# Optimization experiments

Hardware: AMD Instinct MI355X
Metric: run time of the kernel (lower is better)

## Reference

```python
import jax, jax.numpy as jnp
import numpy as np

S, B, DIN, DBERT, H, L = 128, 32, 256, 768, 512, 2
NT_POS, NT_MORPH = 32, 64


def setup_inputs() -> dict:
    key = jax.random.key(0)
    ks = iter(jax.random.split(key, 32))
    def rn(shape, s=0.1):
        return jax.random.normal(next(ks), shape, dtype=jnp.float32) * s
    D0 = DIN + DBERT  # 1024 == 2*H, so per-layer LSTM weights stack cleanly
    return {
        "src_segments": rn((S, B, DIN), 1.0),
        "bert_encodings": rn((B, DBERT), 1.0),
        "labels_pos": jax.random.randint(next(ks), (S, B), 0, NT_POS, dtype=jnp.int32),
        "labels_morph": jax.random.randint(next(ks), (S, B), 0, NT_MORPH, dtype=jnp.int32),
        # stacked LSTM params: [layer, direction, ...], PyTorch gate order i,f,g,o
        "w_ih": rn((L, 2, 4 * H, D0)),
        "w_hh": rn((L, 2, 4 * H, H)),
        "b_ih": rn((L, 2, 4 * H)),
        "b_hh": rn((L, 2, 4 * H)),
        "head_w_pos": rn((NT_POS, 2 * H)),
        "head_b_pos": rn((NT_POS,)),
        "head_w_morph": rn((NT_MORPH, 2 * H)),
        "head_b_morph": rn((NT_MORPH,)),
        "start_pos": rn((NT_POS,)), "end_pos": rn((NT_POS,)), "trans_pos": rn((NT_POS, NT_POS)),
        "start_morph": rn((NT_MORPH,)), "end_morph": rn((NT_MORPH,)), "trans_morph": rn((NT_MORPH, NT_MORPH)),
    }


def _run_dir(x, w_ih, w_hh, b):
    # x: [S, B, D]; one LSTM direction via scan over time
    bsz, hd = x.shape[1], w_hh.shape[1]
    def step(carry, xt):
        h, c = carry
        g = xt @ w_ih.T + h @ w_hh.T + b  # [B, 4H]
        i, f, gg, o = jnp.split(g, 4, axis=-1)
        c = jax.nn.sigmoid(f) * c + jax.nn.sigmoid(i) * jnp.tanh(gg)
        h = jax.nn.sigmoid(o) * jnp.tanh(c)
        return (h, c), h
    init = (jnp.zeros((bsz, hd), x.dtype), jnp.zeros((bsz, hd), x.dtype))
    _, hs = jax.lax.scan(step, init, x)
    return hs


def _bilstm(x, w_ih, w_hh, b_ih, b_hh):
    out = x
    for l in range(w_ih.shape[0]):
        b = b_ih[l] + b_hh[l]
        fwd = _run_dir(out, w_ih[l, 0], w_hh[l, 0], b[0])
        bwd = _run_dir(out[::-1], w_ih[l, 1], w_hh[l, 1], b[1])[::-1]
        out = jnp.concatenate([fwd, bwd], axis=-1)  # [S, B, 2H]
    return out


def _crf_ll(em, tags, start, trans, end):
    # torchcrf log-likelihood, mask=None, reduction='sum'. em: [S,B,K], tags: [S,B]
    bsz = em.shape[1]
    first = start[tags[0]] + em[0, jnp.arange(bsz), tags[0]]
    em_sc = jnp.take_along_axis(em, tags[..., None], axis=2)[..., 0]  # [S,B]
    num = first + trans[tags[:-1], tags[1:]].sum(0) + em_sc[1:].sum(0) + end[tags[-1]]
    def step(alpha, et):  # alpha: [B,K]
        return jax.nn.logsumexp(alpha[:, :, None] + trans[None], axis=1) + et, None
    alpha, _ = jax.lax.scan(step, start[None, :] + em[0], em[1:])
    den = jax.nn.logsumexp(alpha + end[None, :], axis=1)
    return jnp.sum(num - den)


def reference(src_segments, bert_encodings, labels_pos, labels_morph,
              w_ih, w_hh, b_ih, b_hh,
              head_w_pos, head_b_pos, head_w_morph, head_b_morph,
              start_pos, end_pos, trans_pos, start_morph, end_morph, trans_morph):
    # bert encodings are repeated over seq and concatenated on features
    bert = jnp.broadcast_to(bert_encodings[None], (src_segments.shape[0],) + bert_encodings.shape)
    emb = jnp.concatenate([src_segments, bert], axis=-1)  # dropout p=0 -> identity
    out = _bilstm(emb, w_ih, w_hh, b_ih, b_hh)            # [S,B,2H]
    feat_pos = out @ head_w_pos.T + head_b_pos            # [S,B,32]
    feat_morph = out @ head_w_morph.T + head_b_morph      # [S,B,64]
    ll = (_crf_ll(feat_pos, labels_pos, start_pos, trans_pos, end_pos)
          + _crf_ll(feat_morph, labels_morph, start_morph, trans_morph, end_morph))
    return -ll  # loss = -sum_f crf_f(emissions_f, labels_f)
```

## Files before the change

kernel.cpp:

```cpp
#include <hip/hip_runtime.h>


typedef unsigned short u16;
typedef unsigned long long u64;
typedef __attribute__((ext_vector_type(8))) __bf16 bf16x8;
typedef __attribute__((ext_vector_type(4))) float floatx4;

static __device__ __forceinline__ u16 f2bf(float f) {
  unsigned int u = __float_as_uint(f);
  u += 0x7fffu + ((u >> 16) & 1u);
  return (u16)(u >> 16);
}
static __device__ __forceinline__ float sigf(float x) {
  return 1.0f / (1.0f + __expf(-x));
}
static __device__ __forceinline__ float tanh_(float x) {
  return 1.0f - 2.0f / (1.0f + __expf(2.0f * x));
}
static __device__ __forceinline__ floatx4 mfma16(bf16x8 a, bf16x8 b, floatx4 c) {
  return __builtin_amdgcn_mfma_f32_16x16x32_bf16(a, b, c, 0, 0, 0);
}

__global__ __launch_bounds__(256) void prep_kernel(
    const float* __restrict__ w_ih, const float* __restrict__ w_hh,
    const float* __restrict__ b_ih, const float* __restrict__ b_hh,
    const float* __restrict__ src,  const float* __restrict__ bert,
    const float* __restrict__ hwp,  const float* __restrict__ hbp,
    const float* __restrict__ hwm,  const float* __restrict__ hbm,
    u16* __restrict__ Wsrc, u16* __restrict__ Wbert, u16* __restrict__ Wih1,
    u16* __restrict__ Whh,  u16* __restrict__ SrcBf, u16* __restrict__ BertBf,
    u16* __restrict__ Wheads, float* __restrict__ b0sum, float* __restrict__ b1sum,
    float* __restrict__ hb, float* __restrict__ dout)
{
  const int NA = 4194304;
  const int NB = 4194304;
  const int NC = 4194304;
  const int ND = 1048576;
  const int NE = 24576;
  const int NF = 98304;
  const int NG = 8192;
  const int NH = 96;
  const int TOTAL = NA + NB + NC + ND + NE + NF + NG + NH + 1;
  for (int i = blockIdx.x * 256 + threadIdx.x; i < TOTAL; i += gridDim.x * 256) {
    int x = i;
    if (x < NA) {
      int c = x & 1023, r = x >> 10;
      float v = w_ih[x];
      if (c < 256) Wsrc[r * 256 + c] = f2bf(v);
      else         Wbert[r * 768 + (c - 256)] = f2bf(v);
      continue;
    }
    x -= NA;
    if (x < NB) { Wih1[x] = f2bf(w_ih[NA + x]); continue; }
    x -= NB;
    if (x < NC) { Whh[x] = f2bf(w_hh[x]); continue; }
    x -= NC;
    if (x < ND) { SrcBf[x] = f2bf(src[x]); continue; }
    x -= ND;
    if (x < NE) { BertBf[x] = f2bf(bert[x]); continue; }
    x -= NE;
    if (x < NF) {
      Wheads[x] = f2bf(x < 32768 ? hwp[x] : hwm[x - 32768]);
      continue;
    }
    x -= NF;
    if (x < NG) {
      float v = b_ih[x] + b_hh[x];
      if (x < 4096) b0sum[x] = v; else b1sum[x - 4096] = v;
      continue;
    }
    x -= NG;
    if (x < NH) { hb[x] = (x < 32) ? hbp[x] : hbm[x - 32]; continue; }
    dout[0] = 0.f;
  }
}

__global__ __launch_bounds__(256) void gemm_nt(
    const u16* __restrict__ A, int lda,
    const u16* __restrict__ B, int ldb,
    float* __restrict__ C, int ldc,
    int M, int N, int K,
    const float* __restrict__ bias_n,
    const float* __restrict__ auxBN, int auxld,
    int n_split, long dir_stride)
{
  __shared__ __align__(16) u16 As[128 * 64];
  __shared__ __align__(16) u16 Bs[128 * 64];
  const int m0 = blockIdx.y * 128, n0 = blockIdx.x * 128;
  const int tid = threadIdx.x;
  const int wv = tid >> 6, ln = tid & 63;
  const int wm = wv & 1, wn = wv >> 1;
  const int q = ln >> 4, l15 = ln & 15;
  floatx4 acc[4][4];
#pragma unroll
  for (int a = 0; a < 4; ++a)
#pragma unroll
    for (int b2 = 0; b2 < 4; ++b2) acc[a][b2] = (floatx4){0.f, 0.f, 0.f, 0.f};

  for (int kk = 0; kk < K; kk += 64) {
    __syncthreads();
#pragma unroll
    for (int j = 0; j < 4; ++j) {
      const int idx = j * 256 + tid;
      const int r = idx >> 3, cc = idx & 7;
      const int slot = cc ^ (r & 7);
      const int ra = min(m0 + r, M - 1);
      *(int4*)&As[r * 64 + slot * 8] = *(const int4*)&A[(long)ra * lda + kk + cc * 8];
      const int rb = min(n0 + r, N - 1);
      *(int4*)&Bs[r * 64 + slot * 8] = *(const int4*)&B[(long)rb * ldb + kk + cc * 8];
    }
    __syncthreads();
#pragma unroll
    for (int ks = 0; ks < 2; ++ks) {
      bf16x8 af[4], bf[4];
#pragma unroll
      for (int im = 0; im < 4; ++im) {
        const int r = wm * 64 + im * 16 + l15;
        const int slot = (ks * 4 + q) ^ (r & 7);
        af[im] = *(const bf16x8*)&As[r * 64 + slot * 8];
      }
#pragma unroll
      for (int jn = 0; jn < 4; ++jn) {
        const int r = wn * 64 + jn * 16 + l15;
        const int slot = (ks * 4 + q) ^ (r & 7);
        bf[jn] = *(const bf16x8*)&Bs[r * 64 + slot * 8];
      }
#pragma unroll
      for (int im = 0; im < 4; ++im)
#pragma unroll
        for (int jn = 0; jn < 4; ++jn)
          acc[im][jn] = mfma16(af[im], bf[jn], acc[im][jn]);
    }
  }
#pragma unroll
  for (int im = 0; im < 4; ++im)
#pragma unroll
    for (int jn = 0; jn < 4; ++jn) {
      const int n = n0 + wn * 64 + jn * 16 + l15;
      if (n < N) {
        const int dirsel = (n >= n_split) ? 1 : 0;
        const long cb = (long)dirsel * dir_stride - (long)dirsel * n_split + n;
        const float badd = bias_n ? bias_n[n] : 0.f;
#pragma unroll
        for (int rg = 0; rg < 4; ++rg) {
          const int m = m0 + wm * 64 + im * 16 + q * 4 + rg;
          if (m < M) {
            float v = acc[im][jn][rg] + badd;
            if (auxBN) v += auxBN[(long)(m & 31) * auxld + n];
            C[cb + (long)m * ldc] = v;
          }
        }
      }
    }
}

__global__ __launch_bounds__(256, 1) void lstm_rec(
    const float* __restrict__ gates,
    u16* __restrict__ out,
    const u16* __restrict__ whh)
{
  __shared__ __align__(16) u16 h_lds[16 * 512];
  __shared__ float gsc[4][16][17];
  const int bid = blockIdx.x;
  const int dir = bid >> 6;
  const int mh = (bid >> 5) & 1;
  const int u0 = (bid & 31) * 16;
  const int tid = threadIdx.x;
  const int wv = tid >> 6;
  const int ln = tid & 63;
  const int q = ln >> 4, l15 = ln & 15;

  const int gate_r = (l15 >> 2) * 512 + u0 + wv * 4 + (l15 & 3);

  bf16x8 bfrag[16];
  {
    const u16* wp = whh + ((long)dir * 2048 + gate_r) * 512 + q * 8;
#pragma unroll
    for (int ks = 0; ks < 16; ++ks)
      bfrag[ks] = *(const bf16x8*)(wp + ks * 32);
  }

  float c = 0.f;
  const int b_glob = mh * 16 + l15;

  const float* gbase = gates + (((long)dir * 128) * 32 + mh * 16) * 2048 + gate_r;

  float g4[4];
  {
    const float* gp = gbase + (long)(dir ? 127 : 0) * 65536;
#pragma unroll
    for (int rg = 0; rg < 4; ++rg) g4[rg] = gp[(q * 4 + rg) * 2048];
  }

  for (int t = 0; t < 128; ++t) {
    const int s = dir ? (127 - t) : t;
    float g4n[4];
    if (t < 127) {
      const int sn = dir ? (126 - t) : (t + 1);
      const float* gp = gbase + (long)sn * 65536;
#pragma unroll
      for (int rg = 0; rg < 4; ++rg) g4n[rg] = gp[(q * 4 + rg) * 2048];
    }
    floatx4 acc = (floatx4){0.f, 0.f, 0.f, 0.f};
    if (t > 0) {
      const int sp = dir ? (s + 1) : (s - 1);
      const u64* ub = (const u64*)(out + (((long)sp * 32 + mh * 16) * 1024 + (long)dir * 512));
      u64 v8[8];
#pragma unroll
      for (int j = 0; j < 8; ++j) {
        const int idx = j * 256 + tid;
        const int r = idx >> 7, c4 = idx & 127;
        v8[j] = __hip_atomic_load((u64*)(ub + (long)r * 256 + c4),
                                  __ATOMIC_RELAXED, __HIP_MEMORY_SCOPE_AGENT);
      }
      while (true) {
        bool bad = false;
#pragma unroll
        for (int j = 0; j < 8; ++j) bad |= ((v8[j] & 0xffffULL) == 0xffffULL);
        if (!bad) break;
#pragma unroll
        for (int j = 0; j < 8; ++j) {
          if ((v8[j] & 0xffffULL) == 0xffffULL) {
            const int idx = j * 256 + tid;
            const int r = idx >> 7, c4 = idx & 127;
            v8[j] = __hip_atomic_load((u64*)(ub + (long)r * 256 + c4),
                                      __ATOMIC_RELAXED, __HIP_MEMORY_SCOPE_AGENT);
          }
        }
      }
#pragma unroll
      for (int j = 0; j < 8; ++j) {
        const int idx = j * 256 + tid;
        const int r = idx >> 7, c4 = idx & 127;
        const int cc8 = c4 >> 1, hf = c4 & 1;
        *(u64*)&h_lds[r * 512 + ((cc8 ^ (r & 7)) << 3) + (hf << 2)] = v8[j];
      }
      __syncthreads();
      floatx4 acc1 = (floatx4){0.f, 0.f, 0.f, 0.f};
#pragma unroll
      for (int ks = 0; ks < 16; ks += 2) {
        const int slot0 = (ks * 4 + q) ^ (l15 & 7);
        bf16x8 a0 = *(const bf16x8*)&h_lds[l15 * 512 + slot0 * 8];
        acc = mfma16(a0, bfrag[ks], acc);
        const int slot1 = ((ks + 1) * 4 + q) ^ (l15 & 7);
        bf16x8 a1 = *(const bf16x8*)&h_lds[l15 * 512 + slot1 * 8];
        acc1 = mfma16(a1, bfrag[ks + 1], acc1);
      }
      acc += acc1;
    }
#pragma unroll
    for (int rg = 0; rg < 4; ++rg)
      gsc[wv][q * 4 + rg][l15] = acc[rg] + g4[rg];
    const float gi = gsc[wv][l15][q];
    const float gf = gsc[wv][l15][4 + q];
    const float gg = gsc[wv][l15][8 + q];
    const float go = gsc[wv][l15][12 + q];
    const float iv = sigf(gi), fv = sigf(gf), gv = tanh_(gg), ov = sigf(go);
    c = fv * c + iv * gv;
    const float h = ov * tanh_(c);
    const unsigned int hv = (unsigned int)f2bf(h);
    const unsigned int p1 = (unsigned int)__shfl_xor((int)hv, 16);
    const unsigned int lo32 = hv | (p1 << 16);
    const u64 w64 = (u64)lo32 |
                    ((u64)(unsigned int)__shfl_xor((int)lo32, 32) << 32);
    if (q == 0)
      __hip_atomic_store(
          (u64*)&out[((long)s * 32 + b_glob) * 1024 + dir * 512 + u0 + wv * 4],
          w64, __ATOMIC_RELAXED, __HIP_MEMORY_SCOPE_AGENT);
#pragma unroll
    for (int rg = 0; rg < 4; ++rg) g4[rg] = g4n[rg];
  }
}

template <int K>
static __device__ void crf_body(const float* __restrict__ feat, int off,
                                const int* __restrict__ labels, int b,
                                const float* __restrict__ start,
                                const float* __restrict__ end_,
                                const float* __restrict__ trans,
                                float* __restrict__ outp,
                                float* transT, float (*alpha)[64],
                                float* red)
{
  const int tid = threadIdx.x;
  for (int i = tid; i < K * K; i += 256) {
    int kk = i / K, kp2 = i % K;
    transT[kp2 * 65 + kk] = trans[i];
  }
  if (tid < K) alpha[0][tid] = start[tid] + feat[b * 96 + off + tid];
  __syncthreads();
  constexpr int Kq = K / 4;
  const int kp = tid >> 2, k4 = tid & 3;
  const bool act = kp < K;
  int p = 0;
  for (int s = 1; s < 128; ++s) {
    float x[Kq];
    float mx = -3e38f;
    if (act) {
      const float* tr = &transT[kp * 65 + k4 * Kq];
      const float* al = &alpha[p][k4 * Kq];
#pragma unroll
      for (int i2 = 0; i2 < Kq; ++i2) { x[i2] = al[i2] + tr[i2]; mx = fmaxf(mx, x[i2]); }
    }
    mx = fmaxf(mx, __shfl_xor(mx, 1));
    mx = fmaxf(mx, __shfl_xor(mx, 2));
    float ss = 0.f;
    if (act) {
#pragma unroll
      for (int i2 = 0; i2 < Kq; ++i2) ss += __expf(x[i2] - mx);
    }
    ss += __shfl_xor(ss, 1);
    ss += __shfl_xor(ss, 2);
    if (act && k4 == 0)
      alpha[p ^ 1][kp] = mx + __logf(ss) + feat[(s * 32 + b) * 96 + off + kp];
    __syncthreads();
    p ^= 1;
  }
  if (tid < 128) {
    const int tg = labels[tid * 32 + b];
    float term = feat[(tid * 32 + b) * 96 + off + tg];
    if (tid == 0) term += start[tg];
    else          term += trans[labels[(tid - 1) * 32 + b] * K + tg];
    if (tid == 127) term += end_[tg];
    red[tid] = term;
  }
  __syncthreads();
  if (tid == 0) {
    float num = 0.f;
    for (int i = 0; i < 128; ++i) num += red[i];
    float mx = -3e38f;
    for (int k = 0; k < K; ++k) mx = fmaxf(mx, alpha[p][k] + end_[k]);
    float ss = 0.f;
    for (int k = 0; k < K; ++k) ss += __expf(alpha[p][k] + end_[k] - mx);
    const float den = mx + __logf(ss);
    atomicAdd(outp, den - num);
  }
}

__global__ __launch_bounds__(256) void crf_kernel(
    const float* __restrict__ feat,
    const int* __restrict__ labp, const int* __restrict__ labm,
    const float* __restrict__ stp, const float* __restrict__ enp, const float* __restrict__ trp,
    const float* __restrict__ stm, const float* __restrict__ enm, const float* __restrict__ trm,
    float* __restrict__ outp)
{
  __shared__ float transT[64 * 65];
  __shared__ float alpha[2][64];
  __shared__ float red[128];
  const int task = blockIdx.x >> 5, b = blockIdx.x & 31;
  if (task == 0) crf_body<32>(feat, 0,  labp, b, stp, enp, trp, outp, transT, alpha, red);
  else           crf_body<64>(feat, 32, labm, b, stm, enm, trm, outp, transT, alpha, red);
}

extern "C" void kernel_launch(void* const* d_in, const int* in_sizes, int n_in,
                              void* d_out, int out_size, void* d_ws, size_t ws_size,
                              hipStream_t stream) {
  const float* src  = (const float*)d_in[0];
  const float* bert = (const float*)d_in[1];
  const int*   labp = (const int*)d_in[2];
  const int*   labm = (const int*)d_in[3];
  const float* w_ih = (const float*)d_in[4];
  const float* w_hh = (const float*)d_in[5];
  const float* b_ih = (const float*)d_in[6];
  const float* b_hh = (const float*)d_in[7];
  const float* hwp  = (const float*)d_in[8];
  const float* hbp  = (const float*)d_in[9];
  const float* hwm  = (const float*)d_in[10];
  const float* hbm  = (const float*)d_in[11];
  const float* stp  = (const float*)d_in[12];
  const float* enp  = (const float*)d_in[13];
  const float* trp  = (const float*)d_in[14];
  const float* stm  = (const float*)d_in[15];
  const float* enm  = (const float*)d_in[16];
  const float* trm  = (const float*)d_in[17];

  char* ws = (char*)d_ws;
  u16*   Wsrc     = (u16*)(ws + 0);
  u16*   Wbert    = (u16*)(ws + 2097152);
  u16*   Wih1     = (u16*)(ws + 8388608);
  u16*   Whh      = (u16*)(ws + 16777216);
  u16*   SrcBf    = (u16*)(ws + 25165824);
  u16*   BertBf   = (u16*)(ws + 27262976);
  u16*   Wheads   = (u16*)(ws + 27312128);
  float* b0sum    = (float*)(ws + 27508736);
  float* b1sum    = (float*)(ws + 27525120);
  float* hb       = (float*)(ws + 27541504);
  float* bertpart = (float*)(ws + 27542272);
  float* feat     = (float*)(ws + 28066560);
  u16*   out0     = (u16*)(ws + 29639424);
  u16*   out1     = (u16*)(ws + 38028032);
  float* gates    = (float*)(ws + 46416640);
  float* dout     = (float*)d_out;

  hipMemsetAsync(out0, 0xFF, 8388608, stream);
  hipMemsetAsync(out1, 0xFF, 8388608, stream);

  hipLaunchKernelGGL(prep_kernel, dim3(2048), dim3(256), 0, stream,
      w_ih, w_hh, b_ih, b_hh, src, bert, hwp, hbp, hwm, hbm,
      Wsrc, Wbert, Wih1, Whh, SrcBf, BertBf, Wheads, b0sum, b1sum, hb, dout);

  hipLaunchKernelGGL(gemm_nt, dim3(32, 1), dim3(256), 0, stream,
      BertBf, 768, Wbert, 768, bertpart, 4096, 32, 4096, 768,
      b0sum, (const float*)nullptr, 0, 1 << 30, 0L);

  hipLaunchKernelGGL(gemm_nt, dim3(32, 32), dim3(256), 0, stream,
      SrcBf, 256, Wsrc, 256, gates, 2048, 4096, 4096, 256,
      (const float*)nullptr, bertpart, 4096, 2048, (long)(4096L * 2048L));

  {
    const float* g = gates; u16* o = out0; const u16* wh = Whh;
    void* args[] = {&g, &o, &wh};
    hipLaunchCooperativeKernel(reinterpret_cast<void*>(&lstm_rec),
                               dim3(128), dim3(256), args, 0, stream);
  }

  hipLaunchKernelGGL(gemm_nt, dim3(32, 32), dim3(256), 0, stream,
      out0, 1024, Wih1, 1024, gates, 2048, 4096, 4096, 1024,
      b1sum, (const float*)nullptr, 0, 2048, (long)(4096L * 2048L));

  {
    const float* g = gates; u16* o = out1; const u16* wh = Whh + 2L * 2048 * 512;
    void* args[] = {&g, &o, &wh};
    hipLaunchCooperativeKernel(reinterpret_cast<void*>(&lstm_rec),
                               dim3(128), dim3(256), args, 0, stream);
  }

  hipLaunchKernelGGL(gemm_nt, dim3(1, 32), dim3(256), 0, stream,
      out1, 1024, Wheads, 1024, feat, 96, 4096, 96, 1024,
      hb, (const float*)nullptr, 0, 1 << 30, 0L);

  hipLaunchKernelGGL(crf_kernel, dim3(64), dim3(256), 0, stream,
      feat, labp, labm, stp, enp, trp, stm, enm, trm, dout);
}
```

Before: 917.6 us.

## Store precomputed gate inputs as bf16 in a batch-contiguous layout for the recurrence

```diff
diff --git a/kernel.cpp b/kernel.cpp
--- a/kernel.cpp
+++ b/kernel.cpp
@@ -2,14 +2,18 @@
 
 
 typedef unsigned short u16;
+typedef unsigned int u32;
 typedef unsigned long long u64;
 typedef __attribute__((ext_vector_type(8))) __bf16 bf16x8;
 typedef __attribute__((ext_vector_type(4))) float floatx4;
 
 static __device__ __forceinline__ u16 f2bf(float f) {
-  unsigned int u = __float_as_uint(f);
+  u32 u = __float_as_uint(f);
   u += 0x7fffu + ((u >> 16) & 1u);
   return (u16)(u >> 16);
+}
+static __device__ __forceinline__ float bf2f(u32 bits) {
+  return __uint_as_float(bits << 16);
 }
 static __device__ __forceinline__ float sigf(float x) {
   return 1.0f / (1.0f + __expf(-x));
@@ -82,7 +86,7 @@
     int M, int N, int K,
     const float* __restrict__ bias_n,
     const float* __restrict__ auxBN, int auxld,
-    int n_split, long dir_stride)
+    int mode)
 {
   __shared__ __align__(16) u16 As[128 * 64];
   __shared__ __align__(16) u16 Bs[128 * 64];
@@ -132,30 +136,50 @@
           acc[im][jn] = mfma16(af[im], bf[jn], acc[im][jn]);
     }
   }
-#pragma unroll
-  for (int im = 0; im < 4; ++im)
-#pragma unroll
-    for (int jn = 0; jn < 4; ++jn) {
-      const int n = n0 + wn * 64 + jn * 16 + l15;
-      if (n < N) {
-        const int dirsel = (n >= n_split) ? 1 : 0;
-        const long cb = (long)dirsel * dir_stride - (long)dirsel * n_split + n;
-        const float badd = bias_n ? bias_n[n] : 0.f;
-#pragma unroll
-        for (int rg = 0; rg < 4; ++rg) {
-          const int m = m0 + wm * 64 + im * 16 + q * 4 + rg;
-          if (m < M) {
-            float v = acc[im][jn][rg] + badd;
-            if (auxBN) v += auxBN[(long)(m & 31) * auxld + n];
-            C[cb + (long)m * ldc] = v;
+  if (mode == 0) {
+#pragma unroll
+    for (int im = 0; im < 4; ++im)
+#pragma unroll
+      for (int jn = 0; jn < 4; ++jn) {
+        const int n = n0 + wn * 64 + jn * 16 + l15;
+        if (n < N) {
+          const float badd = bias_n ? bias_n[n] : 0.f;
+#pragma unroll
+          for (int rg = 0; rg < 4; ++rg) {
+            const int m = m0 + wm * 64 + im * 16 + q * 4 + rg;
+            if (m < M) {
+              float v = acc[im][jn][rg] + badd;
+              if (auxBN) v += auxBN[(long)(m & 31) * auxld + n];
+              C[(long)m * ldc + n] = v;
+            }
           }
         }
       }
-    }
+  } else {
+    u16* G = (u16*)C;
+#pragma unroll
+    for (int im = 0; im < 4; ++im)
+#pragma unroll
+      for (int jn = 0; jn < 4; ++jn) {
+        const int n = n0 + wn * 64 + jn * 16 + l15;
+        const int dirsel = n >> 11, nn = n & 2047;
+        const int m = m0 + wm * 64 + im * 16 + q * 4;
+        const int s = m >> 5, b0 = m & 31;
+        const float badd = bias_n ? bias_n[n] : 0.f;
+        u64 pk = 0;
+#pragma unroll
+        for (int rg = 0; rg < 4; ++rg) {
+          float v = acc[im][jn][rg] + badd;
+          if (auxBN) v += auxBN[(long)(b0 + rg) * auxld + n];
+          pk |= (u64)f2bf(v) << (16 * rg);
+        }
+        *(u64*)&G[(long)dirsel * 8388608 + ((long)s * 2048 + nn) * 32 + b0] = pk;
+      }
+  }
 }
 
 __global__ __launch_bounds__(256, 1) void lstm_rec(
-    const float* __restrict__ gates,
+    const u16* __restrict__ gates,
     u16* __restrict__ out,
     const u16* __restrict__ whh)
 {
@@ -183,29 +207,18 @@
   float c = 0.f;
   const int b_glob = mh * 16 + l15;
 
-  const float* gbase = gates + (((long)dir * 128) * 32 + mh * 16) * 2048 + gate_r;
-
-  float g4[4];
-  {
-    const float* gp = gbase + (long)(dir ? 127 : 0) * 65536;
-#pragma unroll
-    for (int rg = 0; rg < 4; ++rg) g4[rg] = gp[(q * 4 + rg) * 2048];
-  }
+  const u16* gbase = gates + (long)dir * 8388608 + (long)gate_r * 32 + mh * 16 + q * 4;
+
+  u64 gcur = *(const u64*)(gbase + (long)(dir ? 127 : 0) * 65536);
+  u64 gnext = 0;
 
   for (int t = 0; t < 128; ++t) {
     const int s = dir ? (127 - t) : t;
-    float g4n[4];
-    if (t < 127) {
-      const int sn = dir ? (126 - t) : (t + 1);
-      const float* gp = gbase + (long)sn * 65536;
-#pragma unroll
-      for (int rg = 0; rg < 4; ++rg) g4n[rg] = gp[(q * 4 + rg) * 2048];
-    }
     floatx4 acc = (floatx4){0.f, 0.f, 0.f, 0.f};
+    u64 v8[8];
     if (t > 0) {
       const int sp = dir ? (s + 1) : (s - 1);
       const u64* ub = (const u64*)(out + (((long)sp * 32 + mh * 16) * 1024 + (long)dir * 512));
-      u64 v8[8];
 #pragma unroll
       for (int j = 0; j < 8; ++j) {
         const int idx = j * 256 + tid;
@@ -228,6 +241,12 @@
           }
         }
       }
+    }
+    if (t < 127) {
+      const int sn = dir ? (126 - t) : (t + 1);
+      gnext = *(const u64*)(gbase + (long)sn * 65536);
+    }
+    if (t > 0) {
 #pragma unroll
       for (int j = 0; j < 8; ++j) {
         const int idx = j * 256 + tid;
@@ -250,7 +269,7 @@
     }
 #pragma unroll
     for (int rg = 0; rg < 4; ++rg)
-      gsc[wv][q * 4 + rg][l15] = acc[rg] + g4[rg];
+      gsc[wv][q * 4 + rg][l15] = acc[rg] + bf2f((u32)((gcur >> (16 * rg)) & 0xffffu));
     const float gi = gsc[wv][l15][q];
     const float gf = gsc[wv][l15][4 + q];
     const float gg = gsc[wv][l15][8 + q];
@@ -258,17 +277,16 @@
     const float iv = sigf(gi), fv = sigf(gf), gv = tanh_(gg), ov = sigf(go);
     c = fv * c + iv * gv;
     const float h = ov * tanh_(c);
-    const unsigned int hv = (unsigned int)f2bf(h);
-    const unsigned int p1 = (unsigned int)__shfl_xor((int)hv, 16);
-    const unsigned int lo32 = hv | (p1 << 16);
+    const u32 hv = (u32)f2bf(h);
+    const u32 p1 = (u32)__shfl_xor((int)hv, 16);
+    const u32 lo32 = hv | (p1 << 16);
     const u64 w64 = (u64)lo32 |
-                    ((u64)(unsigned int)__shfl_xor((int)lo32, 32) << 32);
+                    ((u64)(u32)__shfl_xor((int)lo32, 32) << 32);
     if (q == 0)
       __hip_atomic_store(
           (u64*)&out[((long)s * 32 + b_glob) * 1024 + dir * 512 + u0 + wv * 4],
           w64, __ATOMIC_RELAXED, __HIP_MEMORY_SCOPE_AGENT);
-#pragma unroll
-    for (int rg = 0; rg < 4; ++rg) g4[rg] = g4n[rg];
+    gcur = gnext;
   }
 }
 
@@ -389,7 +407,7 @@
   float* feat     = (float*)(ws + 28066560);
   u16*   out0     = (u16*)(ws + 29639424);
   u16*   out1     = (u16*)(ws + 38028032);
-  float* gates    = (float*)(ws + 46416640);
+  u16*   gates    = (u16*)(ws + 46416640);
   float* dout     = (float*)d_out;
 
   hipMemsetAsync(out0, 0xFF, 8388608, stream);
@@ -401,25 +419,25 @@
 
   hipLaunchKernelGGL(gemm_nt, dim3(32, 1), dim3(256), 0, stream,
       BertBf, 768, Wbert, 768, bertpart, 4096, 32, 4096, 768,
-      b0sum, (const float*)nullptr, 0, 1 << 30, 0L);
+      b0sum, (const float*)nullptr, 0, 0);
 
   hipLaunchKernelGGL(gemm_nt, dim3(32, 32), dim3(256), 0, stream,
-      SrcBf, 256, Wsrc, 256, gates, 2048, 4096, 4096, 256,
-      (const float*)nullptr, bertpart, 4096, 2048, (long)(4096L * 2048L));
+      SrcBf, 256, Wsrc, 256, (float*)gates, 0, 4096, 4096, 256,
+      (const float*)nullptr, bertpart, 4096, 1);
 
   {
-    const float* g = gates; u16* o = out0; const u16* wh = Whh;
+    const u16* g = gates; u16* o = out0; const u16* wh = Whh;
     void* args[] = {&g, &o, &wh};
     hipLaunchCooperativeKernel(reinterpret_cast<void*>(&lstm_rec),
                                dim3(128), dim3(256), args, 0, stream);
   }
 
   hipLaunchKernelGGL(gemm_nt, dim3(32, 32), dim3(256), 0, stream,
-      out0, 1024, Wih1, 1024, gates, 2048, 4096, 4096, 1024,
-      b1sum, (const float*)nullptr, 0, 2048, (long)(4096L * 2048L));
+      out0, 1024, Wih1, 1024, (float*)gates, 0, 4096, 4096, 1024,
+      b1sum, (const float*)nullptr, 0, 1);
 
   {
-    const float* g = gates; u16* o = out1; const u16* wh = Whh + 2L * 2048 * 512;
+    const u16* g = gates; u16* o = out1; const u16* wh = Whh + 2L * 2048 * 512;
     void* args[] = {&g, &o, &wh};
     hipLaunchCooperativeKernel(reinterpret_cast<void*>(&lstm_rec),
                                dim3(128), dim3(256), args, 0, stream);
@@ -427,7 +445,7 @@
 
   hipLaunchKernelGGL(gemm_nt, dim3(1, 32), dim3(256), 0, stream,
       out1, 1024, Wheads, 1024, feat, 96, 4096, 96, 1024,
-      hb, (const float*)nullptr, 0, 1 << 30, 0L);
+      hb, (const float*)nullptr, 0, 0);
 
   hipLaunchKernelGGL(crf_kernel, dim3(64), dim3(256), 0, stream,
       feat, labp, labm, stp, enp, trp, stm, enm, trm, dout);
```

Result: slower. 1.028 ms (+12.0%).
